# Kernel optimization log

Hardware: AMD Instinct MI355X
Metric: run time of the kernel (lower is better)

Reference implementation:

```python
import jax, jax.numpy as jnp
import numpy as np

GRID_SIZE, K, NUM_EXPERTS = 5, 3, 8
N_MLP, N_KAN = 4, 4
B, D, H, O = 4096, 512, 2048, 512


def _bspline_basis(x, grid, k):
    """Cox-de Boor recursion, vectorized. x: [B, D]; grid: [G]. Returns [B, D, G-k-1]."""
    xe = x[..., None]
    # order-0: indicator of grid interval
    b = ((grid[:-1] <= xe) & (xe < grid[1:])).astype(x.dtype)  # [B, D, G-1]
    for kk in range(1, k + 1):
        t_i = grid[: -(kk + 1)]
        t_ik = grid[kk:-1]
        t_ik1 = grid[kk + 1:]
        t_i1 = grid[1:-kk]
        left = (xe - t_i) / (t_ik - t_i) * b[..., :-1]
        right = (t_ik1 - xe) / (t_ik1 - t_i1) * b[..., 1:]
        b = left + right
    return b


def setup_inputs() -> dict:
    key = jax.random.key(0)
    ks = jax.random.split(key, 8)
    x = jax.random.normal(ks[0], (B, D), dtype=jnp.float32)
    # Router output: binary expert mask; rows with no active group fall back to expert 7
    mask = (jax.random.uniform(ks[1], (B, NUM_EXPERTS)) < 0.3).astype(jnp.float32)
    other = jnp.zeros((NUM_EXPERTS,), jnp.float32).at[7].set(1.0)
    expert_mask = jnp.where(mask.sum(axis=1, keepdims=True) == 0, other[None, :], mask)
    s_d = 1.0 / np.sqrt(D)
    s_h = 1.0 / np.sqrt(H)
    gate_w = jax.random.normal(ks[2], (D, NUM_EXPERTS), jnp.float32) * s_d
    gate_b = jnp.zeros((NUM_EXPERTS,), jnp.float32)
    mlp_w1 = jax.random.normal(ks[3], (N_MLP, D, H), jnp.float32) * s_d
    mlp_b1 = jnp.zeros((N_MLP, H), jnp.float32)
    mlp_w2 = jax.random.normal(ks[4], (N_MLP, H, O), jnp.float32) * s_h
    mlp_b2 = jnp.zeros((N_MLP, O), jnp.float32)
    kan_scaling = jnp.ones((N_KAN, D, O), jnp.float32)
    kan_coeff = jax.random.normal(ks[5], (N_KAN, D, O, GRID_SIZE + K), jnp.float32)
    return dict(x=x, expert_mask=expert_mask, gate_w=gate_w, gate_b=gate_b,
                mlp_w1=mlp_w1, mlp_b1=mlp_b1, mlp_w2=mlp_w2, mlp_b2=mlp_b2,
                kan_scaling=kan_scaling, kan_coeff=kan_coeff)


def reference(x, expert_mask, gate_w, gate_b, mlp_w1, mlp_b1, mlp_w2, mlp_b2,
              kan_scaling, kan_coeff):
    # gate softmax + router mask + renormalize
    gate = jax.nn.softmax(x @ gate_w + gate_b, axis=1)          # [B, E]
    masked = gate * expert_mask
    w = masked / (masked.sum(axis=1, keepdims=True) + 1e-9)      # [B, E]

    # MLP experts (eval mode -> dropout is identity)
    h = jax.nn.relu(jnp.einsum('bd,edh->ebh', x, mlp_w1) + mlp_b1[:, None, :])
    mlp_out = jnp.einsum('ebh,eho->ebo', h, mlp_w2) + mlp_b2[:, None, :]  # [4, B, O]

    # KAN experts: uniform grid extended by k knots each side (spacing 2/grid_size)
    hg = 2.0 / GRID_SIZE
    grid = jnp.arange(GRID_SIZE + 2 * K + 1, dtype=x.dtype) * hg - (1.0 + K * hg)
    basis = _bspline_basis(x, grid, K)                           # [B, D, 8]
    ceff = kan_coeff * kan_scaling[..., None]                    # [4, D, O, 8]
    kan_out = jnp.einsum('big,eiog->ebo', basis, ceff)           # [4, B, O]

    expert_outputs = jnp.concatenate([mlp_out, kan_out], axis=0)  # [8, B, O]
    out = jnp.einsum('ebo,be->bo', expert_outputs, w)             # [B, O]
    return out, expert_mask, w
```

## Files before the change

### kernel.cpp

```cpp
#include <hip/hip_runtime.h>

typedef __attribute__((ext_vector_type(4))) float f32x4;
typedef __attribute__((ext_vector_type(8))) __bf16 bf16x8;
typedef __attribute__((ext_vector_type(4))) unsigned short u16x4;
typedef __attribute__((ext_vector_type(8))) unsigned short u16x8;

#define NB 4096
#define ND 512
#define NH 2048
#define NO 512

__device__ __forceinline__ unsigned short f2bf(float f) {
  unsigned int u = __float_as_uint(f);
  u += 0x7fffu + ((u >> 16) & 1u);
  return (unsigned short)(u >> 16);
}
__device__ __forceinline__ float bf2f(unsigned short u) {
  return __uint_as_float(((unsigned int)u) << 16);
}
__device__ __forceinline__ void gload_lds16(const void* g, void* l) {
  __builtin_amdgcn_global_load_lds(
      (const __attribute__((address_space(1))) unsigned int*)g,
      (__attribute__((address_space(3))) unsigned int*)l, 16, 0, 0);
}

__global__ void gate_kernel(const float* __restrict__ x, const float* __restrict__ emask,
                            const float* __restrict__ gw, const float* __restrict__ gb,
                            float* __restrict__ w_out, float* __restrict__ mask_out) {
  int b = blockIdx.x;
  int lane = threadIdx.x;
  float l8[8] = {0,0,0,0,0,0,0,0};
  const float* xr = x + (size_t)b * ND;
  for (int d = lane; d < ND; d += 64) {
    float xv = xr[d];
    const float* g = gw + d * 8;
#pragma unroll
    for (int e = 0; e < 8; ++e) l8[e] = fmaf(xv, g[e], l8[e]);
  }
#pragma unroll
  for (int off = 32; off > 0; off >>= 1) {
#pragma unroll
    for (int e = 0; e < 8; ++e) l8[e] += __shfl_xor(l8[e], off);
  }
  float m = -1e30f;
#pragma unroll
  for (int e = 0; e < 8; ++e) { l8[e] += gb[e]; m = fmaxf(m, l8[e]); }
  float s = 0.f, p[8];
#pragma unroll
  for (int e = 0; e < 8; ++e) { p[e] = expf(l8[e] - m); s += p[e]; }
  float inv = 1.f / s;
  float mk[8], me[8], ms = 0.f;
#pragma unroll
  for (int e = 0; e < 8; ++e) {
    mk[e] = emask[(size_t)b * 8 + e];
    me[e] = p[e] * inv * mk[e];
    ms += me[e];
  }
  float winv = 1.f / (ms + 1e-9f);
  if (lane == 0) {
#pragma unroll
    for (int e = 0; e < 8; ++e) {
      w_out[(size_t)b * 8 + e] = me[e] * winv;
      mask_out[(size_t)b * 8 + e] = mk[e];
    }
  }
}

__global__ void cast_x_kernel(const float* __restrict__ x, unsigned short* __restrict__ xb) {
  size_t i = ((size_t)blockIdx.x * 256 + threadIdx.x) * 4;
  f32x4 v = *(const f32x4*)(x + i);
  u16x4 r;
#pragma unroll
  for (int j = 0; j < 4; ++j) r[j] = f2bf(v[j]);
  *(u16x4*)(xb + i) = r;
}

__global__ void basis_kernel(const float* __restrict__ x, unsigned short* __restrict__ bas) {
  size_t t = (size_t)blockIdx.x * 256 + threadIdx.x;
  float xv = x[t];
  const float hg = 0.4f;
  float tt[12];
#pragma unroll
  for (int j = 0; j < 12; ++j) tt[j] = -2.2f + hg * (float)j;
  float b0[11];
#pragma unroll
  for (int j = 0; j < 11; ++j) b0[j] = (tt[j] <= xv && xv < tt[j + 1]) ? 1.f : 0.f;
  float b1[10], b2[9], b3[8];
#pragma unroll
  for (int j = 0; j < 10; ++j) b1[j] = ((xv - tt[j]) * b0[j] + (tt[j + 2] - xv) * b0[j + 1]) * (1.f / (1.f * hg));
#pragma unroll
  for (int j = 0; j < 9; ++j)  b2[j] = ((xv - tt[j]) * b1[j] + (tt[j + 3] - xv) * b1[j + 1]) * (1.f / (2.f * hg));
#pragma unroll
  for (int j = 0; j < 8; ++j)  b3[j] = ((xv - tt[j]) * b2[j] + (tt[j + 4] - xv) * b2[j + 1]) * (1.f / (3.f * hg));
  u16x8 r;
#pragma unroll
  for (int j = 0; j < 8; ++j) r[j] = f2bf(b3[j]);
  *(u16x8*)(bas + t * 8) = r;
}

__global__ void transpose_cast(const float* __restrict__ in, unsigned short* __restrict__ outp,
                               int R, int Cc) {
  __shared__ float tile[32][33];
  int e = blockIdx.z;
  int c0 = blockIdx.x * 32, r0 = blockIdx.y * 32;
  int tx = threadIdx.x & 31, ty = threadIdx.x >> 5;
  const float* ine = in + (size_t)e * R * Cc;
  unsigned short* oute = outp + (size_t)e * R * Cc;
#pragma unroll
  for (int j = 0; j < 32; j += 8)
    tile[ty + j][tx] = ine[(size_t)(r0 + ty + j) * Cc + (c0 + tx)];
  __syncthreads();
#pragma unroll
  for (int j = 0; j < 32; j += 8)
    oute[(size_t)(c0 + ty + j) * R + (r0 + tx)] = f2bf(tile[tx][ty + j]);
}

__global__ void make_cefft(const float* __restrict__ coeff, const float* __restrict__ scal,
                           unsigned short* __restrict__ outp) {
  size_t t = (size_t)blockIdx.x * 256 + threadIdx.x;
  int i = (int)(t & 511);
  int o = (int)((t >> 9) & 511);
  int e = (int)(t >> 18);
  size_t io = ((size_t)e * 512 + i) * 512 + o;
  const f32x4* cp = (const f32x4*)(coeff + io * 8);
  f32x4 c0 = cp[0], c1 = cp[1];
  float s = scal[io];
  u16x8 r;
#pragma unroll
  for (int j = 0; j < 4; ++j) r[j] = f2bf(c0[j] * s);
#pragma unroll
  for (int j = 0; j < 4; ++j) r[4 + j] = f2bf(c1[j] * s);
  *(u16x8*)(outp + ((size_t)e * 512 + o) * 4096 + (size_t)i * 8) = r;
}

struct GemmArgs {
  const unsigned short* A; size_t sAe; int lda;
  const unsigned short* B; size_t sBe; int ldb;
  const float* bias; int sBias;
  unsigned short* C; size_t sCe; size_t sHalf; int ldc;
  int Kspan; int zshift; int gx; int nxy;
  int mode;
};

__global__ __launch_bounds__(512, 2) void gemm_fused(int nL1, GemmArgs a1, GemmArgs a2) {
  __shared__ __align__(16) char lsA[3 * 16384];
  __shared__ __align__(16) char lsB[3 * 16384];
  const int wg = blockIdx.x;
  const GemmArgs g = (wg < nL1) ? a1 : a2;
  const int wgl = (wg < nL1) ? wg : wg - nL1;
  const int tid = threadIdx.x;
  const int lane = tid & 63, wid = tid >> 6;
  const int wr = wid >> 2, wc = wid & 3;
  const int z = wgl / g.nxy;
  int rem = wgl % g.nxy;
  rem = (rem & 7) * (g.nxy >> 3) + (rem >> 3);
  const int bcol = (rem % g.gx) * 256;
  const int brow = (rem / g.gx) * 256;
  const int e = z >> g.zshift;
  const int half = z & ((1 << g.zshift) - 1);
  const unsigned short* Ae = g.A + (size_t)e * g.sAe + (size_t)half * g.Kspan;
  const unsigned short* Be = g.B + (size_t)e * g.sBe + (size_t)half * g.Kspan;
  const int lda = g.lda, ldb = g.ldb;
  const int NT = g.Kspan >> 5;

  const int fr = lane & 15, fc = lane >> 4;
  const int sR = tid >> 2, ssc = tid & 3;

  auto stage = [&](int buf, int t2) {
#pragma unroll
    for (int q = 0; q < 2; ++q) {
      int R = q * 128 + sR;
      int kk = t2 * 32 + ((ssc ^ ((R >> 1) & 3)) << 3);
      gload_lds16(Ae + (size_t)(brow + R) * lda + (size_t)kk,
                  lsA + buf * 16384 + q * 8192 + tid * 16);
    }
#pragma unroll
    for (int q = 0; q < 2; ++q) {
      int R = q * 128 + sR;
      int kk = t2 * 32 + ((ssc ^ ((R >> 1) & 3)) << 3);
      gload_lds16(Be + (size_t)(bcol + R) * ldb + (size_t)kk,
                  lsB + buf * 16384 + q * 8192 + tid * 16);
    }
  };

  f32x4 acc[8][4] = {};

  stage(0, 0);
  stage(1, 1);
  asm volatile("s_waitcnt vmcnt(4)" ::: "memory");
  __builtin_amdgcn_s_barrier();

  int bi = 0;
  for (int t = 0; t < NT; ++t) {
    const char* bA = lsA + bi * 16384;
    const char* bB = lsB + bi * 16384;
    const int pb = (bi == 0) ? 2 : bi - 1;
    const bool pf = (t + 2 < NT);

    bf16x8 af[8], bfrag[4];
#pragma unroll
    for (int i = 0; i < 8; ++i) {
      int ra = wr * 128 + i * 16 + fr;
      af[i] = *(const bf16x8*)(bA + ra * 64 + ((fc ^ ((ra >> 1) & 3)) << 4));
    }
#pragma unroll
    for (int n = 0; n < 4; ++n) {
      int rb = wc * 64 + n * 16 + fr;
      bfrag[n] = *(const bf16x8*)(bB + rb * 64 + ((fc ^ ((rb >> 1) & 3)) << 4));
    }
    if (pf) stage(pb, t + 2);
    __builtin_amdgcn_s_barrier();
    asm volatile("s_waitcnt lgkmcnt(0)" ::: "memory");
    __builtin_amdgcn_sched_barrier(0);
    __builtin_amdgcn_s_setprio(1);
#pragma unroll
    for (int mi = 0; mi < 8; ++mi)
#pragma unroll
      for (int ni = 0; ni < 4; ++ni)
        acc[mi][ni] = __builtin_amdgcn_mfma_f32_16x16x32_bf16(bfrag[ni], af[mi], acc[mi][ni], 0, 0, 0);
    __builtin_amdgcn_s_setprio(0);
    if (pf)               asm volatile("s_waitcnt vmcnt(4)" ::: "memory");
    else if (t + 1 < NT)  asm volatile("s_waitcnt vmcnt(0)" ::: "memory");
    __builtin_amdgcn_s_barrier();

    bi = (bi == 2) ? 0 : bi + 1;
  }

  unsigned short* Ce = g.C + (size_t)e * g.sCe + (size_t)half * g.sHalf;
  const int ldc = g.ldc;
#pragma unroll
  for (int mi = 0; mi < 8; ++mi) {
    int row = brow + wr * 128 + mi * 16 + fr;
#pragma unroll
    for (int ni = 0; ni < 4; ++ni) {
      int col0 = bcol + wc * 64 + ni * 16 + (fc << 2);
      u16x4 r;
      if (g.mode == 0) {
        f32x4 bv = *(const f32x4*)(g.bias + e * g.sBias + col0);
#pragma unroll
        for (int j = 0; j < 4; ++j) r[j] = f2bf(fmaxf(acc[mi][ni][j] + bv[j], 0.f));
      } else {
#pragma unroll
        for (int j = 0; j < 4; ++j) r[j] = f2bf(acc[mi][ni][j]);
      }
      *(u16x4*)(Ce + (size_t)row * ldc + col0) = r;
    }
  }
}

__global__ void combine_kernel(const unsigned short* __restrict__ eoM,
                               const unsigned short* __restrict__ eoK,
                               const float* __restrict__ b2,
                               const float* __restrict__ w, float* __restrict__ out) {
  int b = blockIdx.x;
  int o = threadIdx.x * 4;
  float wv[8];
#pragma unroll
  for (int e = 0; e < 8; ++e) wv[e] = w[(size_t)b * 8 + e];
  f32x4 acc = {0.f, 0.f, 0.f, 0.f};
#pragma unroll
  for (int e = 0; e < 4; ++e) {
    u16x4 m0 = *(const u16x4*)(eoM + ((size_t)e * NB + b) * NO + o);
    u16x4 m1 = *(const u16x4*)(eoM + ((size_t)(4 + e) * NB + b) * NO + o);
    f32x4 bb = *(const f32x4*)(b2 + e * NO + o);
#pragma unroll
    for (int j = 0; j < 4; ++j)
      acc[j] = fmaf(wv[e], bf2f(m0[j]) + bf2f(m1[j]) + bb[j], acc[j]);
  }
#pragma unroll
  for (int e = 0; e < 4; ++e) {
    u16x4 k0 = *(const u16x4*)(eoK + ((size_t)e * NB + b) * NO + o);
    u16x4 k1 = *(const u16x4*)(eoK + ((size_t)(4 + e) * NB + b) * NO + o);
#pragma unroll
    for (int j = 0; j < 4; ++j)
      acc[j] = fmaf(wv[4 + e], bf2f(k0[j]) + bf2f(k1[j]), acc[j]);
  }
  *(f32x4*)(out + (size_t)b * NO + o) = acc;
}

extern "C" void kernel_launch(void* const* d_in, const int* in_sizes, int n_in,
                              void* d_out, int out_size, void* d_ws, size_t ws_size,
                              hipStream_t stream) {
  (void)in_sizes; (void)n_in; (void)out_size;
  const float* x      = (const float*)d_in[0];
  const float* emask  = (const float*)d_in[1];
  const float* gate_w = (const float*)d_in[2];
  const float* gate_b = (const float*)d_in[3];
  const float* mlp_w1 = (const float*)d_in[4];
  const float* mlp_b1 = (const float*)d_in[5];
  const float* mlp_w2 = (const float*)d_in[6];
  const float* mlp_b2 = (const float*)d_in[7];
  const float* kan_s  = (const float*)d_in[8];
  const float* kan_c  = (const float*)d_in[9];

  float* out = (float*)d_out;
  float* mask_out = out + (size_t)NB * NO;
  float* w_out    = mask_out + (size_t)NB * 8;

  char* ws = (char*)d_ws;
  size_t off = 0;
  auto take = [&](size_t bytes) { size_t r = off; off += (bytes + 255) & ~(size_t)255; return r; };
  unsigned short* w1t   = (unsigned short*)(ws + take((size_t)4 * NH * ND * 2));
  unsigned short* w2t   = (unsigned short*)(ws + take((size_t)4 * NO * NH * 2));
  unsigned short* cefft = (unsigned short*)(ws + take((size_t)4 * NO * (ND * 8) * 2));
  unsigned short* xbf   = (unsigned short*)(ws + take((size_t)NB * ND * 2));
  unsigned short* regA  = (unsigned short*)(ws + take((size_t)8 * NB * NO * 2));
  unsigned short* hbuf  = (unsigned short*)(ws + take((size_t)4 * NB * NH * 2));
  size_t base_need = off;
  size_t eoK_off = base_need;
  const bool fused = (ws_size >= base_need + (size_t)8 * NB * NO * 2);
  unsigned short* eoM = regA;
  unsigned short* bas, *eoK;
  if (fused) {
    bas = regA;
    eoK = (unsigned short*)(ws + eoK_off);
  } else {
    bas = hbuf;
    eoK = (unsigned short*)((char*)hbuf + (size_t)2 * NB * NH * 2);
  }

  gate_kernel<<<NB, 64, 0, stream>>>(x, emask, gate_w, gate_b, w_out, mask_out);
  cast_x_kernel<<<(NB * ND) / (256 * 4), 256, 0, stream>>>(x, xbf);
  transpose_cast<<<dim3(NH / 32, ND / 32, 4), 256, 0, stream>>>(mlp_w1, w1t, ND, NH);
  transpose_cast<<<dim3(NO / 32, NH / 32, 4), 256, 0, stream>>>(mlp_w2, w2t, NH, NO);
  make_cefft<<<(4 * ND * NO) / 256, 256, 0, stream>>>(kan_c, kan_s, cefft);

  GemmArgs aL1 = { xbf, 0, ND,
                   w1t, (size_t)NH * ND, ND,
                   mlp_b1, NH,
                   hbuf, (size_t)NB * NH, 0, NH,
                   ND, 0, NH / 256, (NH / 256) * (NB / 256), 0 };
  GemmArgs aL2 = { hbuf, (size_t)NB * NH, NH,
                   w2t, (size_t)NO * NH, NH,
                   nullptr, 0,
                   eoM, (size_t)NB * NO, (size_t)4 * NB * NO, NO,
                   NH / 2, 1, NO / 256, (NO / 256) * (NB / 256), 2 };
  GemmArgs aL3 = { bas, 0, ND * 8,
                   cefft, (size_t)NO * (ND * 8), ND * 8,
                   nullptr, 0,
                   eoK, (size_t)NB * NO, (size_t)4 * NB * NO, NO,
                   (ND * 8) / 2, 1, NO / 256, (NO / 256) * (NB / 256), 2 };

  if (fused) {
    basis_kernel<<<(NB * ND) / 256, 256, 0, stream>>>(x, bas);
    gemm_fused<<<512 + 256, 512, 0, stream>>>(512, aL1, aL3);
    gemm_fused<<<256, 512, 0, stream>>>(0, aL2, aL2);
  } else {
    gemm_fused<<<512, 512, 0, stream>>>(512, aL1, aL1);
    gemm_fused<<<256, 512, 0, stream>>>(0, aL2, aL2);
    basis_kernel<<<(NB * ND) / 256, 256, 0, stream>>>(x, bas);
    gemm_fused<<<256, 512, 0, stream>>>(0, aL3, aL3);
  }

  combine_kernel<<<NB, NO / 4, 0, stream>>>(eoM, eoK, mlp_b2, w_out, out);
}
```

Measured before the change: 233.0 us.

## Pre-tile GEMM operands into K-blocked swizzled layout for contiguous LDS staging

All GEMM operands (x, basis, transposed weights, KAN coefficients, hidden activations) are now written by their producer kernels into a layout blocked by 32-wide K tiles, with the XOR swizzle already applied. Each 32-element K slab of consecutive rows is contiguous, so the GEMM's global-to-LDS loads read one contiguous block per tile instead of strided row segments. This aims to improve memory coalescing and lower address arithmetic in the main GEMMs. In exchange the producer kernels do scattered writes, and every producer and consumer has to agree on the new addressing.

```diff
diff --git a/kernel.cpp b/kernel.cpp
--- a/kernel.cpp
+++ b/kernel.cpp
@@ -22,6 +22,10 @@
   __builtin_amdgcn_global_load_lds(
       (const __attribute__((address_space(1))) unsigned int*)g,
       (__attribute__((address_space(3))) unsigned int*)l, 16, 0, 0);
+}
+__device__ __forceinline__ size_t paddr(int row, int k, int Mtot) {
+  int kt = k >> 5, c = (k >> 3) & 3, el = k & 7;
+  return ((size_t)kt * Mtot + row) * 32 + (size_t)((c ^ ((row >> 1) & 3)) * 8 + el);
 }
 
 __global__ void gate_kernel(const float* __restrict__ x, const float* __restrict__ emask,
@@ -67,16 +71,21 @@
 }
 
 __global__ void cast_x_kernel(const float* __restrict__ x, unsigned short* __restrict__ xb) {
-  size_t i = ((size_t)blockIdx.x * 256 + threadIdx.x) * 4;
-  f32x4 v = *(const f32x4*)(x + i);
-  u16x4 r;
-#pragma unroll
-  for (int j = 0; j < 4; ++j) r[j] = f2bf(v[j]);
-  *(u16x4*)(xb + i) = r;
+  size_t t = (size_t)blockIdx.x * 256 + threadIdx.x;
+  int b = (int)(t >> 6);
+  int k0 = ((int)t & 63) * 8;
+  const f32x4* px = (const f32x4*)(x + (size_t)b * ND + k0);
+  f32x4 v0 = px[0], v1 = px[1];
+  u16x8 r;
+#pragma unroll
+  for (int j = 0; j < 4; ++j) { r[j] = f2bf(v0[j]); r[4 + j] = f2bf(v1[j]); }
+  *(u16x8*)(xb + paddr(b, k0, NB)) = r;
 }
 
 __global__ void basis_kernel(const float* __restrict__ x, unsigned short* __restrict__ bas) {
   size_t t = (size_t)blockIdx.x * 256 + threadIdx.x;
+  int b = (int)(t >> 9);
+  int i = (int)(t & 511);
   float xv = x[t];
   const float hg = 0.4f;
   float tt[12];
@@ -95,7 +104,7 @@
   u16x8 r;
 #pragma unroll
   for (int j = 0; j < 8; ++j) r[j] = f2bf(b3[j]);
-  *(u16x8*)(bas + t * 8) = r;
+  *(u16x8*)(bas + paddr(b, i * 8, NB)) = r;
 }
 
 __global__ void transpose_cast(const float* __restrict__ in, unsigned short* __restrict__ outp,
@@ -112,7 +121,7 @@
   __syncthreads();
 #pragma unroll
   for (int j = 0; j < 32; j += 8)
-    oute[(size_t)(c0 + ty + j) * R + (r0 + tx)] = f2bf(tile[tx][ty + j]);
+    oute[paddr(c0 + ty + j, r0 + tx, Cc)] = f2bf(tile[tx][ty + j]);
 }
 
 __global__ void make_cefft(const float* __restrict__ coeff, const float* __restrict__ scal,
@@ -130,12 +139,12 @@
   for (int j = 0; j < 4; ++j) r[j] = f2bf(c0[j] * s);
 #pragma unroll
   for (int j = 0; j < 4; ++j) r[4 + j] = f2bf(c1[j] * s);
-  *(u16x8*)(outp + ((size_t)e * 512 + o) * 4096 + (size_t)i * 8) = r;
+  *(u16x8*)(outp + (size_t)e * NO * (ND * 8) + paddr(o, i * 8, NO)) = r;
 }
 
 struct GemmArgs {
-  const unsigned short* A; size_t sAe; int lda;
-  const unsigned short* B; size_t sBe; int ldb;
+  const unsigned short* A; size_t sAe; int Ma;
+  const unsigned short* B; size_t sBe; int Mb;
   const float* bias; int sBias;
   unsigned short* C; size_t sCe; size_t sHalf; int ldc;
   int Kspan; int zshift; int gx; int nxy;
@@ -158,9 +167,10 @@
   const int brow = (rem / g.gx) * 256;
   const int e = z >> g.zshift;
   const int half = z & ((1 << g.zshift) - 1);
-  const unsigned short* Ae = g.A + (size_t)e * g.sAe + (size_t)half * g.Kspan;
-  const unsigned short* Be = g.B + (size_t)e * g.sBe + (size_t)half * g.Kspan;
-  const int lda = g.lda, ldb = g.ldb;
+  const int ktBase = half * (g.Kspan >> 5);
+  const unsigned short* Ae = g.A + (size_t)e * g.sAe;
+  const unsigned short* Be = g.B + (size_t)e * g.sBe;
+  const int Ma = g.Ma, Mb = g.Mb;
   const int NT = g.Kspan >> 5;
 
   const int fr = lane & 15, fc = lane >> 4;
@@ -169,17 +179,15 @@
   auto stage = [&](int buf, int t2) {
 #pragma unroll
     for (int q = 0; q < 2; ++q) {
-      int R = q * 128 + sR;
-      int kk = t2 * 32 + ((ssc ^ ((R >> 1) & 3)) << 3);
-      gload_lds16(Ae + (size_t)(brow + R) * lda + (size_t)kk,
-                  lsA + buf * 16384 + q * 8192 + tid * 16);
+      const unsigned short* src =
+          Ae + ((size_t)(ktBase + t2) * Ma + (brow + q * 128 + sR)) * 32 + ssc * 8;
+      gload_lds16(src, lsA + buf * 16384 + q * 8192 + tid * 16);
     }
 #pragma unroll
     for (int q = 0; q < 2; ++q) {
-      int R = q * 128 + sR;
-      int kk = t2 * 32 + ((ssc ^ ((R >> 1) & 3)) << 3);
-      gload_lds16(Be + (size_t)(bcol + R) * ldb + (size_t)kk,
-                  lsB + buf * 16384 + q * 8192 + tid * 16);
+      const unsigned short* src =
+          Be + ((size_t)(ktBase + t2) * Mb + (bcol + q * 128 + sR)) * 32 + ssc * 8;
+      gload_lds16(src, lsB + buf * 16384 + q * 8192 + tid * 16);
     }
   };
 
@@ -239,11 +247,12 @@
         f32x4 bv = *(const f32x4*)(g.bias + e * g.sBias + col0);
 #pragma unroll
         for (int j = 0; j < 4; ++j) r[j] = f2bf(fmaxf(acc[mi][ni][j] + bv[j], 0.f));
+        *(u16x4*)(Ce + paddr(row, col0, NB)) = r;
       } else {
 #pragma unroll
         for (int j = 0; j < 4; ++j) r[j] = f2bf(acc[mi][ni][j]);
+        *(u16x4*)(Ce + (size_t)row * ldc + col0) = r;
       }
-      *(u16x4*)(Ce + (size_t)row * ldc + col0) = r;
     }
   }
 }
@@ -320,23 +329,23 @@
   }
 
   gate_kernel<<<NB, 64, 0, stream>>>(x, emask, gate_w, gate_b, w_out, mask_out);
-  cast_x_kernel<<<(NB * ND) / (256 * 4), 256, 0, stream>>>(x, xbf);
+  cast_x_kernel<<<(NB * ND / 8) / 256, 256, 0, stream>>>(x, xbf);
   transpose_cast<<<dim3(NH / 32, ND / 32, 4), 256, 0, stream>>>(mlp_w1, w1t, ND, NH);
   transpose_cast<<<dim3(NO / 32, NH / 32, 4), 256, 0, stream>>>(mlp_w2, w2t, NH, NO);
   make_cefft<<<(4 * ND * NO) / 256, 256, 0, stream>>>(kan_c, kan_s, cefft);
 
-  GemmArgs aL1 = { xbf, 0, ND,
-                   w1t, (size_t)NH * ND, ND,
+  GemmArgs aL1 = { xbf, 0, NB,
+                   w1t, (size_t)NH * ND, NH,
                    mlp_b1, NH,
                    hbuf, (size_t)NB * NH, 0, NH,
                    ND, 0, NH / 256, (NH / 256) * (NB / 256), 0 };
-  GemmArgs aL2 = { hbuf, (size_t)NB * NH, NH,
-                   w2t, (size_t)NO * NH, NH,
+  GemmArgs aL2 = { hbuf, (size_t)NB * NH, NB,
+                   w2t, (size_t)NO * NH, NO,
                    nullptr, 0,
                    eoM, (size_t)NB * NO, (size_t)4 * NB * NO, NO,
                    NH / 2, 1, NO / 256, (NO / 256) * (NB / 256), 2 };
-  GemmArgs aL3 = { bas, 0, ND * 8,
-                   cefft, (size_t)NO * (ND * 8), ND * 8,
+  GemmArgs aL3 = { bas, 0, NB,
+                   cefft, (size_t)NO * (ND * 8), NO,
                    nullptr, 0,
                    eoK, (size_t)NB * NO, (size_t)4 * NB * NO, NO,
                    (ND * 8) / 2, 1, NO / 256, (NO / 256) * (NB / 256), 2 };
```

Result: faster. 223.9 us (-3.9%).
